# Kernel tuning notes

Hardware: AMD Instinct MI355X
Metric: run time of the kernel (lower is better)

The kernel has to match this reference:

```python
import jax, jax.numpy as jnp
import numpy as np

# env_params constants (chosen, see shape_source)
ETN, EAN = 64, 64          # entity type / attribute nums
RTN, RAN = 128, 64         # relationship type / attribute nums
ME, MR = 2048, 65536       # max entities / relationships
TES, THM, HID = 16, 256, 128
ENV = ETN + RTN + TES      # 208 = GRU input size


def _lin(key, out_d, in_d):
    k1, k2 = jax.random.split(key)
    lim = 1.0 / np.sqrt(in_d)
    W = jax.random.uniform(k1, (out_d, in_d), minval=-lim, maxval=lim, dtype=jnp.float32)
    b = jax.random.uniform(k2, (out_d,), minval=-lim, maxval=lim, dtype=jnp.float32)
    return W, b


def setup_inputs() -> dict:
    key = jax.random.key(0)
    ks = jax.random.split(key, 32)
    # entity: one-hot type in cols [0:ETN], random attributes after
    etype = jax.nn.one_hot(jax.random.randint(ks[0], (ME,), 0, ETN), ETN, dtype=jnp.float32)
    entity = jnp.concatenate([etype, jax.random.normal(ks[1], (ME, EAN), jnp.float32)], axis=1)
    rtype = jax.nn.one_hot(jax.random.randint(ks[2], (MR,), 0, RTN), RTN, dtype=jnp.float32)
    relationship = jnp.concatenate([rtype, jax.random.normal(ks[3], (MR, RAN + ME), jnp.float32)], axis=1)
    target = jax.random.normal(ks[4], (ME + EAN + MR + RAN,), jnp.float32)
    action_mask = (jax.random.uniform(ks[5], (THM,)) > 0.2).astype(jnp.float32)
    # entity encoder: 128 -> 32 -> 8 -> 1
    ew1, eb1 = _lin(ks[6], 32, ETN + EAN)
    ew2, eb2 = _lin(ks[7], 8, 32)
    ew3, eb3 = _lin(ks[8], 1, 8)
    # relationship encoder: 2240 -> 128 -> 64 -> 32 -> 8 -> 1
    rin = RTN + RAN + ME
    rw1, rb1 = _lin(ks[9], 128, rin)
    rw2, rb2 = _lin(ks[10], 64, 128)
    rw3, rb3 = _lin(ks[11], 32, 64)
    rw4, rb4 = _lin(ks[12], 8, 32)
    rw5, rb5 = _lin(ks[13], 1, 8)
    # target encoder: 67712 -> 64 -> 16
    tin = ME + EAN + MR + RAN
    tw1, tb1 = _lin(ks[14], 64, tin)
    tw2, tb2 = _lin(ks[15], TES, 64)
    # GRUCell(208, 128)
    lim = 1.0 / np.sqrt(HID)
    wih = jax.random.uniform(ks[16], (3 * HID, ENV), minval=-lim, maxval=lim, dtype=jnp.float32)
    whh = jax.random.uniform(ks[17], (3 * HID, HID), minval=-lim, maxval=lim, dtype=jnp.float32)
    bih = jax.random.uniform(ks[18], (3 * HID,), minval=-lim, maxval=lim, dtype=jnp.float32)
    bhh = jax.random.uniform(ks[19], (3 * HID,), minval=-lim, maxval=lim, dtype=jnp.float32)
    hidden = jax.random.normal(ks[20], (1, HID), jnp.float32)
    aw, ab = _lin(ks[21], THM, HID)
    return dict(entity=entity, relationship=relationship, target=target, action_mask=action_mask,
                ew1=ew1, eb1=eb1, ew2=ew2, eb2=eb2, ew3=ew3, eb3=eb3,
                rw1=rw1, rb1=rb1, rw2=rw2, rb2=rb2, rw3=rw3, rb3=rb3, rw4=rw4, rb4=rb4, rw5=rw5, rb5=rb5,
                tw1=tw1, tb1=tb1, tw2=tw2, tb2=tb2,
                wih=wih, whh=whh, bih=bih, bhh=bhh, hidden=hidden, aw=aw, ab=ab)


def _masked_group_max(onehot_mask, feat):
    # onehot_mask: [N, T] (==1 where row belongs to type t); feat: [N, 1]
    m = onehot_mask == 1.0
    vals = jnp.max(jnp.where(m, feat, -jnp.inf), axis=0)      # [T]
    return jnp.where(jnp.any(m, axis=0), vals, 0.0)            # empty group -> 0


def reference(entity, relationship, target, action_mask,
              ew1, eb1, ew2, eb2, ew3, eb3,
              rw1, rb1, rw2, rb2, rw3, rb3, rw4, rb4, rw5, rb5,
              tw1, tb1, tw2, tb2,
              wih, whh, bih, bhh, hidden, aw, ab):
    relu = jax.nn.relu
    # entity encoder -> [ME, 1]
    ef = relu(entity @ ew1.T + eb1)
    ef = relu(ef @ ew2.T + eb2)
    ef = ef @ ew3.T + eb3
    # relationship encoder -> [MR, 1]
    rf = relu(relationship @ rw1.T + rb1)
    rf = relu(rf @ rw2.T + rb2)
    rf = relu(rf @ rw3.T + rb3)
    rf = relu(rf @ rw4.T + rb4)
    rf = rf @ rw5.T + rb5
    # one-hot masked segment max over type columns
    eg = _masked_group_max(entity[:, :ETN], ef)          # [ETN]
    rg = _masked_group_max(relationship[:, :RTN], rf)    # [RTN]
    # target encoder -> [TES]
    tf = relu(target @ tw1.T + tb1) @ tw2.T + tb2
    env = jnp.concatenate([eg, rg, tf]).reshape(1, ENV)
    # GRUCell (torch gate order: r, z, n)
    gx = env @ wih.T + bih
    gh = hidden @ whh.T + bhh
    xr, xz, xn = jnp.split(gx, 3, axis=1)
    hr, hz, hn = jnp.split(gh, 3, axis=1)
    r = jax.nn.sigmoid(xr + hr)
    z = jax.nn.sigmoid(xz + hz)
    n = jnp.tanh(xn + r * hn)
    h = ((1.0 - z) * n + z * hidden).reshape(-1)         # [128]
    logits = jax.nn.softmax(h @ aw.T + ab, axis=0)       # [THM]
    return logits * action_mask
```

## Files before the change

### kernel.cpp

```cpp
#include <hip/hip_runtime.h>
#include <stdint.h>

typedef unsigned short u16;
typedef short s16x8 __attribute__((ext_vector_type(8)));
typedef float f32x4 __attribute__((ext_vector_type(4)));

__device__ __forceinline__ float bf2f(u16 u) {
  union { unsigned u; float f; } c; c.u = ((unsigned)u) << 16; return c.f;
}
__device__ __forceinline__ u16 f2bf(float f) {
  union { float f; unsigned u; } c; c.f = f;
  unsigned r = c.u + 0x7FFFu + ((c.u >> 16) & 1u);
  return (u16)(r >> 16);
}
__device__ __forceinline__ unsigned encf(float x) {
  union { float f; unsigned u; } c; c.f = x;
  return (c.u & 0x80000000u) ? ~c.u : (c.u | 0x80000000u);
}
__device__ __forceinline__ float decf(unsigned e) {
  union { unsigned u; float f; } c;
  c.u = (e & 0x80000000u) ? (e ^ 0x80000000u) : ~e;
  return c.f;
}
__device__ __forceinline__ f32x4 mfma16(s16x8 a, s16x8 b, f32x4 c) {
  return __builtin_amdgcn_mfma_f32_16x16x32_bf16(a, b, c, 0, 0, 0);
}
__device__ __forceinline__ float relu(float x) { return x > 0.f ? x : 0.f; }

template <int F32>
__device__ __forceinline__ void loadf8(const void* p, size_t ei, float* o) {
  if (F32) {
    const float* f = (const float*)p + ei;
    f32x4 a = *(const f32x4*)f;
    f32x4 b = *(const f32x4*)(f + 4);
#pragma unroll
    for (int j = 0; j < 4; ++j) { o[j] = a[j]; o[4 + j] = b[j]; }
  } else {
    s16x8 v = *(const s16x8*)((const u16*)p + ei);
#pragma unroll
    for (int j = 0; j < 8; ++j) o[j] = bf2f((u16)v[j]);
  }
}
template <int F32>
__device__ __forceinline__ s16x8 load8b(const void* p, size_t ei) {
  if (F32) {
    float o[8]; loadf8<1>(p, ei, o);
    s16x8 r;
#pragma unroll
    for (int j = 0; j < 8; ++j) r[j] = (short)f2bf(o[j]);
    return r;
  } else {
    return *(const s16x8*)((const u16*)p + ei);
  }
}
template <int F32>
__device__ __forceinline__ float ld1(const void* p, size_t ei) {
  return F32 ? ((const float*)p)[ei] : bf2f(((const u16*)p)[ei]);
}

__global__ void k_detect(const u16* __restrict__ entity, const u16* __restrict__ rel,
                         unsigned* __restrict__ ws) {
  __shared__ unsigned cnt[256];
  const int t = threadIdx.x;
  ws[t] = 0u;
  unsigned c = 0;
  for (int i = t; i < 16384; i += 256) {
    unsigned u = rel[i];
    if ((u & 0x7F80u) == 0x7F80u) ++c;
  }
  for (int i = t; i < 8192; i += 256) {
    unsigned u = entity[i];
    if ((u & 0x7F80u) == 0x7F80u) ++c;
  }
  cnt[t] = c;
  __syncthreads();
  for (int st = 128; st > 0; st >>= 1) {
    if (t < st) cnt[t] += cnt[t + st];
    __syncthreads();
  }
  if (t == 0) ws[256] = cnt[0] ? 1u : 0u;
}

template <int F32>
__global__ __launch_bounds__(256) void k_ent(
    const void* __restrict__ entity, const void* __restrict__ ew1, const void* __restrict__ eb1,
    const void* __restrict__ ew2, const void* __restrict__ eb2,
    const void* __restrict__ ew3, const void* __restrict__ eb3,
    unsigned* __restrict__ egws, const unsigned* __restrict__ flag) {
  if (*flag != (unsigned)F32) return;
  __shared__ __align__(16) u16 xl[32 * 136];
  __shared__ __align__(16) u16 w1l[32 * 136];
  __shared__ float h1l[32 * 33];
  __shared__ float h2l[32 * 9];
  const int t = threadIdx.x;
  const int row0 = blockIdx.x * 32;
#pragma unroll
  for (int p = 0; p < 2; ++p) {
    int lin = p * 256 + t, rr = lin >> 4, cc = lin & 15;
    *(s16x8*)(xl + rr * 136 + cc * 8) =
        load8b<F32>(entity, (size_t)(row0 + rr) * 128 + cc * 8);
    *(s16x8*)(w1l + rr * 136 + cc * 8) = load8b<F32>(ew1, (size_t)rr * 128 + cc * 8);
  }
  __syncthreads();
  {
    const int r = t >> 3, g = t & 7;
    float acc[4] = {0.f, 0.f, 0.f, 0.f};
#pragma unroll 4
    for (int c = 0; c < 16; ++c) {
      s16x8 xv = *(const s16x8*)(xl + r * 136 + c * 8);
      float xf[8];
#pragma unroll
      for (int j = 0; j < 8; ++j) xf[j] = bf2f((u16)xv[j]);
#pragma unroll
      for (int s = 0; s < 4; ++s) {
        s16x8 wv = *(const s16x8*)(w1l + (g + 8 * s) * 136 + c * 8);
#pragma unroll
        for (int j = 0; j < 8; ++j) acc[s] += xf[j] * bf2f((u16)wv[j]);
      }
    }
#pragma unroll
    for (int s = 0; s < 4; ++s)
      h1l[r * 33 + g + 8 * s] = relu(acc[s] + ld1<F32>(eb1, g + 8 * s));
  }
  __syncthreads();
  {
    const int r = t >> 3, o = t & 7;
    float a = ld1<F32>(eb2, o);
#pragma unroll 8
    for (int k = 0; k < 32; ++k) a += h1l[r * 33 + k] * ld1<F32>(ew2, o * 32 + k);
    h2l[r * 9 + o] = relu(a);
  }
  __syncthreads();
  if (t < 32) {
    float s = ld1<F32>(eb3, 0);
#pragma unroll
    for (int k = 0; k < 8; ++k) s += h2l[t * 9 + k] * ld1<F32>(ew3, k);
    int ty = 0;
#pragma unroll
    for (int c = 0; c < 8; ++c) {
      s16x8 v = *(const s16x8*)(xl + t * 136 + c * 8);
#pragma unroll
      for (int j = 0; j < 8; ++j)
        if ((u16)v[j] == (u16)0x3F80) ty = c * 8 + j;
    }
    atomicMax(egws + ty, encf(s));
  }
}

template <int F32>
__global__ __launch_bounds__(256) void k_tgt(const void* __restrict__ target,
                                             const void* __restrict__ tw1,
                                             float* __restrict__ tpart,
                                             const unsigned* __restrict__ flag) {
  if (*flag != (unsigned)F32) return;
  __shared__ float red[256];
  const int t = threadIdx.x;
  const int o = blockIdx.x >> 2, c = blockIdx.x & 3;
  float a = 0.f;
  for (int i = t; i < 2116; i += 256) {
    float xf[8], wf[8];
    loadf8<F32>(target, (size_t)c * 16928 + i * 8, xf);
    loadf8<F32>(tw1, (size_t)o * 67712 + c * 16928 + i * 8, wf);
#pragma unroll
    for (int j = 0; j < 8; ++j) a += xf[j] * wf[j];
  }
  red[t] = a;
  __syncthreads();
  for (int st = 128; st > 0; st >>= 1) {
    if (t < st) red[t] += red[t + st];
    __syncthreads();
  }
  if (t == 0) atomicAdd(tpart + o, red[0]);
}

#define RK 2240
template <int F32>
__global__ __launch_bounds__(256) void k_rel(
    const void* __restrict__ rel, const void* __restrict__ rw1, const void* __restrict__ rb1,
    const void* __restrict__ rw2, const void* __restrict__ rb2,
    const void* __restrict__ rw3, const void* __restrict__ rb3,
    const void* __restrict__ rw4, const void* __restrict__ rb4,
    const void* __restrict__ rw5, const void* __restrict__ rb5,
    unsigned* __restrict__ rgws, const unsigned* __restrict__ flag) {
  if (*flag != (unsigned)F32) return;
  __shared__ __align__(16) unsigned char sm[53760];
  u16* smA = (u16*)sm;
  u16* smB = (u16*)(sm + 8192);
  u16* r0 = (u16*)sm;
  u16* smRF = (u16*)(sm + 18432);
  int* styp = (int*)(sm + 53248);

  const int t = threadIdx.x;
  const int lane = t & 63;
  const int wid = t >> 6;
  const int row0 = blockIdx.x * 128;
  const int fr = lane & 15, fq = lane >> 4;

  if (t < 128) {
    int ty = 0;
#pragma unroll 4
    for (int c = 0; c < 16; ++c) {
      s16x8 v = load8b<F32>(rel, (size_t)(row0 + t) * RK + c * 8);
#pragma unroll
      for (int j = 0; j < 8; ++j)
        if ((u16)v[j] == (u16)0x3F80) ty = c * 8 + j;
    }
    styp[t] = ty;
  }

  const int wm = wid >> 1, wn = wid & 1;
  f32x4 acc[4][4];
#pragma unroll
  for (int i = 0; i < 4; ++i)
#pragma unroll
    for (int j = 0; j < 4; ++j) acc[i][j] = f32x4{0.f, 0.f, 0.f, 0.f};

  const size_t gA0 = (size_t)(row0 + (t >> 2)) * RK + (t & 3) * 8;
  const size_t gB0 = (size_t)(t >> 2) * RK + (t & 3) * 8;

  for (int ki = 0; ki < 70; ++ki) {
    const int k0 = ki * 32;
    s16x8 va0 = load8b<F32>(rel, gA0 + k0);
    s16x8 va1 = load8b<F32>(rel, gA0 + (size_t)64 * RK + k0);
    s16x8 vb0 = load8b<F32>(rw1, gB0 + k0);
    s16x8 vb1 = load8b<F32>(rw1, gB0 + (size_t)64 * RK + k0);
    __syncthreads();
    *(s16x8*)(smA + t * 8) = va0;
    *(s16x8*)(smA + 2048 + t * 8) = va1;
    *(s16x8*)(smB + t * 8) = vb0;
    *(s16x8*)(smB + 2048 + t * 8) = vb1;
    __syncthreads();
    s16x8 a[4], b[4];
#pragma unroll
    for (int i = 0; i < 4; ++i)
      a[i] = *(const s16x8*)(smA + (wm * 64 + i * 16 + fr) * 32 + fq * 8);
#pragma unroll
    for (int j = 0; j < 4; ++j)
      b[j] = *(const s16x8*)(smB + (wn * 64 + j * 16 + fr) * 32 + fq * 8);
#pragma unroll
    for (int i = 0; i < 4; ++i)
#pragma unroll
      for (int j = 0; j < 4; ++j) acc[i][j] = mfma16(a[i], b[j], acc[i][j]);
  }
  __syncthreads();

#pragma unroll
  for (int j = 0; j < 4; ++j) {
    const int col = wn * 64 + j * 16 + fr;
    const float bias = ld1<F32>(rb1, col);
#pragma unroll
    for (int i = 0; i < 4; ++i) {
      const int rbase = wm * 64 + i * 16 + fq * 4;
#pragma unroll
      for (int r = 0; r < 4; ++r)
        smRF[(rbase + r) * 136 + col] = f2bf(relu(acc[i][j][r] + bias));
    }
  }
  __syncthreads();

  if (t < 128) {
    const u16* rfrow = smRF + t * 136;
    for (int o = 0; o < 64; ++o) {
      float a = ld1<F32>(rb2, o);
      for (int k = 0; k < 128; k += 8) {
        float wf[8];
        loadf8<F32>(rw2, o * 128 + k, wf);
#pragma unroll
        for (int j = 0; j < 8; ++j) a += bf2f(rfrow[k + j]) * wf[j];
      }
      r0[t * 72 + o] = f2bf(relu(a));
    }
    const u16* h2row = r0 + t * 72;
    float h3[32];
#pragma unroll
    for (int o = 0; o < 32; ++o) {
      float a = ld1<F32>(rb3, o);
      for (int k = 0; k < 64; k += 8) {
        float wf[8];
        loadf8<F32>(rw3, o * 64 + k, wf);
#pragma unroll
        for (int j = 0; j < 8; ++j) a += bf2f(h2row[k + j]) * wf[j];
      }
      h3[o] = relu(a);
    }
    float h4[8];
#pragma unroll
    for (int o = 0; o < 8; ++o) {
      float a = ld1<F32>(rb4, o);
#pragma unroll
      for (int k = 0; k < 32; ++k) a += h3[k] * ld1<F32>(rw4, o * 32 + k);
      h4[o] = relu(a);
    }
    float s = ld1<F32>(rb5, 0);
#pragma unroll
    for (int k = 0; k < 8; ++k) s += h4[k] * ld1<F32>(rw5, k);
    atomicMax(rgws + styp[t], encf(s));
  }
}

__global__ __launch_bounds__(256, 2) void k_relf(
    const float* __restrict__ rel, const float* __restrict__ rw1, const float* __restrict__ rb1,
    const float* __restrict__ rw2, const float* __restrict__ rb2,
    const float* __restrict__ rw3, const float* __restrict__ rb3,
    const float* __restrict__ rw4, const float* __restrict__ rb4,
    const float* __restrict__ rw5, const float* __restrict__ rb5,
    unsigned* __restrict__ rgws, const unsigned* __restrict__ flag) {
  if (*flag != 1u) return;
  __shared__ __align__(16) unsigned char sm[53760];
  u16* r0 = (u16*)sm;
  u16* smRF = (u16*)(sm + 18432);

  const int t = threadIdx.x;
  const int lane = t & 63;
  const int wid = t >> 6;
  const int row0 = blockIdx.x * 128;
  const int fr = lane & 15, fq = lane >> 4;
  const int wm = wid >> 1, wn = wid & 1;

  int ty = 0;
  if (t < 128) {
    const float* rrow = rel + (size_t)(row0 + t) * RK;
#pragma unroll 8
    for (int c = 0; c < 128; c += 4) {
      f32x4 v = *(const f32x4*)(rrow + c);
#pragma unroll
      for (int j = 0; j < 4; ++j)
        if (v[j] == 1.0f) ty = c + j;
    }
  }

  f32x4 acc[4][4];
#pragma unroll
  for (int i = 0; i < 4; ++i)
#pragma unroll
    for (int j = 0; j < 4; ++j) acc[i][j] = f32x4{0.f, 0.f, 0.f, 0.f};

  const float* pa[4];
  const float* pb[4];
#pragma unroll
  for (int i = 0; i < 4; ++i) {
    pa[i] = rel + (size_t)(row0 + wm * 64 + i * 16 + fr) * RK + fq * 8;
    pb[i] = rw1 + (size_t)(wn * 64 + i * 16 + fr) * RK + fq * 8;
  }

#pragma unroll 2
  for (int ki = 0; ki < 70; ++ki) {
    f32x4 ar[4][2], br[4][2];
#pragma unroll
    for (int i = 0; i < 4; ++i) {
      ar[i][0] = *(const f32x4*)pa[i];
      ar[i][1] = *(const f32x4*)(pa[i] + 4);
      br[i][0] = *(const f32x4*)pb[i];
      br[i][1] = *(const f32x4*)(pb[i] + 4);
      pa[i] += 32;
      pb[i] += 32;
    }
    s16x8 af[4], bg[4];
#pragma unroll
    for (int i = 0; i < 4; ++i) {
#pragma unroll
      for (int e = 0; e < 4; ++e) {
        af[i][e] = (short)f2bf(ar[i][0][e]);
        af[i][4 + e] = (short)f2bf(ar[i][1][e]);
        bg[i][e] = (short)f2bf(br[i][0][e]);
        bg[i][4 + e] = (short)f2bf(br[i][1][e]);
      }
    }
#pragma unroll
    for (int i = 0; i < 4; ++i)
#pragma unroll
      for (int j = 0; j < 4; ++j) acc[i][j] = mfma16(af[i], bg[j], acc[i][j]);
  }

#pragma unroll
  for (int j = 0; j < 4; ++j) {
    const int col = wn * 64 + j * 16 + fr;
    const float bias = rb1[col];
#pragma unroll
    for (int i = 0; i < 4; ++i) {
      const int rbase = wm * 64 + i * 16 + fq * 4;
#pragma unroll
      for (int r = 0; r < 4; ++r)
        smRF[(rbase + r) * 136 + col] = f2bf(relu(acc[i][j][r] + bias));
    }
  }
  __syncthreads();

  if (t < 128) {
    const u16* rfrow = smRF + t * 136;
    for (int o = 0; o < 64; ++o) {
      float a = rb2[o];
      for (int k = 0; k < 128; k += 8) {
        f32x4 w0 = *(const f32x4*)(rw2 + o * 128 + k);
        f32x4 w1 = *(const f32x4*)(rw2 + o * 128 + k + 4);
#pragma unroll
        for (int j = 0; j < 4; ++j) {
          a += bf2f(rfrow[k + j]) * w0[j];
          a += bf2f(rfrow[k + 4 + j]) * w1[j];
        }
      }
      r0[t * 72 + o] = f2bf(relu(a));
    }
    const u16* h2row = r0 + t * 72;
    float h3[32];
#pragma unroll
    for (int o = 0; o < 32; ++o) {
      float a = rb3[o];
      for (int k = 0; k < 64; k += 8) {
        f32x4 w0 = *(const f32x4*)(rw3 + o * 64 + k);
        f32x4 w1 = *(const f32x4*)(rw3 + o * 64 + k + 4);
#pragma unroll
        for (int j = 0; j < 4; ++j) {
          a += bf2f(h2row[k + j]) * w0[j];
          a += bf2f(h2row[k + 4 + j]) * w1[j];
        }
      }
      h3[o] = relu(a);
    }
    float h4[8];
#pragma unroll
    for (int o = 0; o < 8; ++o) {
      float a = rb4[o];
#pragma unroll
      for (int k = 0; k < 32; ++k) a += h3[k] * rw4[o * 32 + k];
      h4[o] = relu(a);
    }
    float s = rb5[0];
#pragma unroll
    for (int k = 0; k < 8; ++k) s += h4[k] * rw5[k];
    atomicMax(rgws + ty, encf(s));
  }
}

template <int F32>
__global__ __launch_bounds__(256) void k_fin(
    const unsigned* __restrict__ egws, const unsigned* __restrict__ rgws,
    const float* __restrict__ tpart, const void* __restrict__ tb1,
    const void* __restrict__ tw2, const void* __restrict__ tb2,
    const void* __restrict__ wih, const void* __restrict__ whh,
    const void* __restrict__ bih, const void* __restrict__ bhh,
    const void* __restrict__ hidden, const void* __restrict__ aw,
    const void* __restrict__ ab, const void* __restrict__ amask,
    void* __restrict__ outp, const unsigned* __restrict__ flag) {
  if (*flag != (unsigned)F32) return;
  __shared__ float env[208];
  __shared__ float th1[64];
  __shared__ float gx[384], gh[384];
  __shared__ float hv[128], hid[128];
  __shared__ float red[256];
  const int t = threadIdx.x;
  if (t < 64) {
    unsigned e = egws[t];
    env[t] = e ? decf(e) : 0.f;
    th1[t] = relu(tpart[t] + ld1<F32>(tb1, t));
  }
  if (t >= 64 && t < 192) {
    unsigned e = rgws[t - 64];
    env[t] = e ? decf(e) : 0.f;
  }
  if (t < 128) hid[t] = ld1<F32>(hidden, t);
  __syncthreads();
  if (t < 16) {
    float a = ld1<F32>(tb2, t);
    for (int k = 0; k < 64; k += 8) {
      float wf[8];
      loadf8<F32>(tw2, t * 64 + k, wf);
#pragma unroll
      for (int j = 0; j < 8; ++j) a += th1[k + j] * wf[j];
    }
    env[192 + t] = a;
  }
  __syncthreads();
  for (int o = t; o < 384; o += 256) {
    float ax = ld1<F32>(bih, o);
#pragma unroll 2
    for (int c = 0; c < 26; ++c) {
      float wf[8];
      loadf8<F32>(wih, (size_t)o * 208 + c * 8, wf);
#pragma unroll
      for (int j = 0; j < 8; ++j) ax += env[c * 8 + j] * wf[j];
    }
    gx[o] = ax;
    float ah = ld1<F32>(bhh, o);
#pragma unroll 2
    for (int c = 0; c < 16; ++c) {
      float wf[8];
      loadf8<F32>(whh, (size_t)o * 128 + c * 8, wf);
#pragma unroll
      for (int j = 0; j < 8; ++j) ah += hid[c * 8 + j] * wf[j];
    }
    gh[o] = ah;
  }
  __syncthreads();
  if (t < 128) {
    float r = 1.f / (1.f + expf(-(gx[t] + gh[t])));
    float z = 1.f / (1.f + expf(-(gx[128 + t] + gh[128 + t])));
    float n = tanhf(gx[256 + t] + r * gh[256 + t]);
    hv[t] = (1.f - z) * n + z * hid[t];
  }
  __syncthreads();
  float s = ld1<F32>(ab, t);
#pragma unroll 4
  for (int c = 0; c < 16; ++c) {
    float wf[8];
    loadf8<F32>(aw, (size_t)t * 128 + c * 8, wf);
#pragma unroll
    for (int j = 0; j < 8; ++j) s += hv[c * 8 + j] * wf[j];
  }
  red[t] = s;
  __syncthreads();
  for (int st = 128; st > 0; st >>= 1) {
    if (t < st) red[t] = fmaxf(red[t], red[t + st]);
    __syncthreads();
  }
  float m = red[0];
  __syncthreads();
  float e = expf(s - m);
  red[t] = e;
  __syncthreads();
  for (int st = 128; st > 0; st >>= 1) {
    if (t < st) red[t] += red[t + st];
    __syncthreads();
  }
  float v = e * (1.f / red[0]) * ld1<F32>(amask, t);
  if (F32) ((float*)outp)[t] = v;
  else ((u16*)outp)[t] = f2bf(v);
}

extern "C" void kernel_launch(void* const* d_in, const int* in_sizes, int n_in,
                              void* d_out, int out_size, void* d_ws, size_t ws_size,
                              hipStream_t stream) {
  const void* entity = d_in[0];
  const void* rel    = d_in[1];
  const void* target = d_in[2];
  const void* amask  = d_in[3];
  const void* ew1 = d_in[4];  const void* eb1 = d_in[5];
  const void* ew2 = d_in[6];  const void* eb2 = d_in[7];
  const void* ew3 = d_in[8];  const void* eb3 = d_in[9];
  const void* rw1 = d_in[10]; const void* rb1 = d_in[11];
  const void* rw2 = d_in[12]; const void* rb2 = d_in[13];
  const void* rw3 = d_in[14]; const void* rb3 = d_in[15];
  const void* rw4 = d_in[16]; const void* rb4 = d_in[17];
  const void* rw5 = d_in[18]; const void* rb5 = d_in[19];
  const void* tw1 = d_in[20]; const void* tb1 = d_in[21];
  const void* tw2 = d_in[22]; const void* tb2 = d_in[23];
  const void* wih = d_in[24]; const void* whh = d_in[25];
  const void* bih = d_in[26]; const void* bhh = d_in[27];
  const void* hidden = d_in[28];
  const void* aw = d_in[29];  const void* ab = d_in[30];

  unsigned* ws = (unsigned*)d_ws;
  unsigned* egws = ws;
  unsigned* rgws = ws + 64;
  float* tpart = (float*)(ws + 192);
  const unsigned* flag = ws + 256;

  hipLaunchKernelGGL(k_detect, dim3(1), dim3(256), 0, stream,
                     (const u16*)entity, (const u16*)rel, ws);

  hipLaunchKernelGGL((k_ent<0>), dim3(64), dim3(256), 0, stream,
                     entity, ew1, eb1, ew2, eb2, ew3, eb3, egws, flag);
  hipLaunchKernelGGL((k_ent<1>), dim3(64), dim3(256), 0, stream,
                     entity, ew1, eb1, ew2, eb2, ew3, eb3, egws, flag);

  hipLaunchKernelGGL((k_tgt<0>), dim3(256), dim3(256), 0, stream, target, tw1, tpart, flag);
  hipLaunchKernelGGL((k_tgt<1>), dim3(256), dim3(256), 0, stream, target, tw1, tpart, flag);

  hipLaunchKernelGGL((k_rel<0>), dim3(512), dim3(256), 0, stream,
                     rel, rw1, rb1, rw2, rb2, rw3, rb3, rw4, rb4, rw5, rb5, rgws, flag);
  hipLaunchKernelGGL(k_relf, dim3(512), dim3(256), 0, stream,
                     (const float*)rel, (const float*)rw1, (const float*)rb1,
                     (const float*)rw2, (const float*)rb2, (const float*)rw3,
                     (const float*)rb3, (const float*)rw4, (const float*)rb4,
                     (const float*)rw5, (const float*)rb5, rgws, flag);

  hipLaunchKernelGGL((k_fin<0>), dim3(1), dim3(256), 0, stream,
                     egws, rgws, tpart, tb1, tw2, tb2, wih, whh, bih, bhh,
                     hidden, aw, ab, amask, d_out, flag);
  hipLaunchKernelGGL((k_fin<1>), dim3(1), dim3(256), 0, stream,
                     egws, rgws, tpart, tb1, tw2, tb2, wih, whh, bih, bhh,
                     hidden, aw, ab, amask, d_out, flag);
}
```

Measured before the change: 1.287 ms.

## Stage fp32 relationship GEMM tiles through double-buffered LDS as bf16

The fp32 relationship encoder kernel now has each thread load a contiguous 16-float chunk of A and B per K step, convert it to bf16 once, and store it into a double-buffered shared-memory tile. MFMA fragments are then read from LDS rather than each wave loading and converting its own strided global fragments. This removes redundant global loads and conversions across waves and lets the next tile's loads overlap the current tile's MFMAs. Type detection now reuses the staged bf16 tiles from the first four K steps instead of a separate global scan. The cost is more LDS per block and a barrier on every K step.

```diff
diff --git a/kernel.cpp b/kernel.cpp
--- a/kernel.cpp
+++ b/kernel.cpp
@@ -26,6 +26,15 @@
   return __builtin_amdgcn_mfma_f32_16x16x32_bf16(a, b, c, 0, 0, 0);
 }
 __device__ __forceinline__ float relu(float x) { return x > 0.f ? x : 0.f; }
+__device__ __forceinline__ s16x8 cvt8(f32x4 a, f32x4 b) {
+  s16x8 r;
+#pragma unroll
+  for (int e = 0; e < 4; ++e) {
+    r[e] = (short)f2bf(a[e]);
+    r[4 + e] = (short)f2bf(b[e]);
+  }
+  return r;
+}
 
 template <int F32>
 __device__ __forceinline__ void loadf8(const void* p, size_t ei, float* o) {
@@ -298,7 +307,7 @@
   }
 }
 
-__global__ __launch_bounds__(256, 2) void k_relf(
+__global__ __launch_bounds__(256, 2) void k_relg(
     const float* __restrict__ rel, const float* __restrict__ rw1, const float* __restrict__ rb1,
     const float* __restrict__ rw2, const float* __restrict__ rb2,
     const float* __restrict__ rw3, const float* __restrict__ rb3,
@@ -306,10 +315,7 @@
     const float* __restrict__ rw5, const float* __restrict__ rb5,
     unsigned* __restrict__ rgws, const unsigned* __restrict__ flag) {
   if (*flag != 1u) return;
-  __shared__ __align__(16) unsigned char sm[53760];
-  u16* r0 = (u16*)sm;
-  u16* smRF = (u16*)(sm + 18432);
-
+  __shared__ __align__(16) unsigned char sm[67584];
   const int t = threadIdx.x;
   const int lane = t & 63;
   const int wid = t >> 6;
@@ -317,61 +323,78 @@
   const int fr = lane & 15, fq = lane >> 4;
   const int wm = wid >> 1, wn = wid & 1;
 
+  const float* pA = rel + (size_t)(row0 + (t >> 1)) * RK + (t & 1) * 16;
+  const float* pB = rw1 + (size_t)(t >> 1) * RK + (t & 1) * 16;
+  const int sidx = 16 * t;
+
+  f32x4 acc[4][4];
+#pragma unroll
+  for (int i = 0; i < 4; ++i)
+#pragma unroll
+    for (int j = 0; j < 4; ++j) acc[i][j] = f32x4{0.f, 0.f, 0.f, 0.f};
+
+  {
+    f32x4 pre[8];
+#pragma unroll
+    for (int q = 0; q < 4; ++q) pre[q] = *(const f32x4*)(pA + q * 4);
+#pragma unroll
+    for (int q = 0; q < 4; ++q) pre[4 + q] = *(const f32x4*)(pB + q * 4);
+    u16* dA = (u16*)sm;
+    u16* dB = (u16*)(sm + 8192);
+    *(s16x8*)(dA + sidx) = cvt8(pre[0], pre[1]);
+    *(s16x8*)(dA + sidx + 8) = cvt8(pre[2], pre[3]);
+    *(s16x8*)(dB + sidx) = cvt8(pre[4], pre[5]);
+    *(s16x8*)(dB + sidx + 8) = cvt8(pre[6], pre[7]);
+  }
+  __syncthreads();
+
   int ty = 0;
-  if (t < 128) {
-    const float* rrow = rel + (size_t)(row0 + t) * RK;
-#pragma unroll 8
-    for (int c = 0; c < 128; c += 4) {
-      f32x4 v = *(const f32x4*)(rrow + c);
-#pragma unroll
-      for (int j = 0; j < 4; ++j)
-        if (v[j] == 1.0f) ty = c + j;
-    }
-  }
-
-  f32x4 acc[4][4];
-#pragma unroll
-  for (int i = 0; i < 4; ++i)
-#pragma unroll
-    for (int j = 0; j < 4; ++j) acc[i][j] = f32x4{0.f, 0.f, 0.f, 0.f};
-
-  const float* pa[4];
-  const float* pb[4];
-#pragma unroll
-  for (int i = 0; i < 4; ++i) {
-    pa[i] = rel + (size_t)(row0 + wm * 64 + i * 16 + fr) * RK + fq * 8;
-    pb[i] = rw1 + (size_t)(wn * 64 + i * 16 + fr) * RK + fq * 8;
-  }
-
-#pragma unroll 2
+#pragma unroll 1
   for (int ki = 0; ki < 70; ++ki) {
-    f32x4 ar[4][2], br[4][2];
-#pragma unroll
-    for (int i = 0; i < 4; ++i) {
-      ar[i][0] = *(const f32x4*)pa[i];
-      ar[i][1] = *(const f32x4*)(pa[i] + 4);
-      br[i][0] = *(const f32x4*)pb[i];
-      br[i][1] = *(const f32x4*)(pb[i] + 4);
-      pa[i] += 32;
-      pb[i] += 32;
-    }
-    s16x8 af[4], bg[4];
-#pragma unroll
-    for (int i = 0; i < 4; ++i) {
-#pragma unroll
-      for (int e = 0; e < 4; ++e) {
-        af[i][e] = (short)f2bf(ar[i][0][e]);
-        af[i][4 + e] = (short)f2bf(ar[i][1][e]);
-        bg[i][e] = (short)f2bf(br[i][0][e]);
-        bg[i][4 + e] = (short)f2bf(br[i][1][e]);
+    const int nk = ki + 1;
+    f32x4 pre[8];
+    if (nk < 70) {
+      const int k0 = nk * 32;
+#pragma unroll
+      for (int q = 0; q < 4; ++q) pre[q] = *(const f32x4*)(pA + k0 + q * 4);
+#pragma unroll
+      for (int q = 0; q < 4; ++q) pre[4 + q] = *(const f32x4*)(pB + k0 + q * 4);
+    }
+    const u16* bA = (const u16*)(sm + (ki & 1) * 16384);
+    const u16* bB = (const u16*)(sm + (ki & 1) * 16384 + 8192);
+    s16x8 a[4], b[4];
+#pragma unroll
+    for (int i = 0; i < 4; ++i)
+      a[i] = *(const s16x8*)(bA + (wm * 64 + i * 16 + fr) * 32 + fq * 8);
+#pragma unroll
+    for (int j = 0; j < 4; ++j)
+      b[j] = *(const s16x8*)(bB + (wn * 64 + j * 16 + fr) * 32 + fq * 8);
+#pragma unroll
+    for (int i = 0; i < 4; ++i)
+#pragma unroll
+      for (int j = 0; j < 4; ++j) acc[i][j] = mfma16(a[i], b[j], acc[i][j]);
+    if (ki < 4 && t < 128) {
+#pragma unroll
+      for (int c = 0; c < 4; ++c) {
+        s16x8 v = *(const s16x8*)(bA + t * 32 + c * 8);
+#pragma unroll
+        for (int j = 0; j < 8; ++j)
+          if ((u16)v[j] == (u16)0x3F80) ty = ki * 32 + c * 8 + j;
       }
     }
-#pragma unroll
-    for (int i = 0; i < 4; ++i)
-#pragma unroll
-      for (int j = 0; j < 4; ++j) acc[i][j] = mfma16(af[i], bg[j], acc[i][j]);
-  }
-
+    if (nk < 70) {
+      u16* dA = (u16*)(sm + (nk & 1) * 16384);
+      u16* dB = (u16*)(sm + (nk & 1) * 16384 + 8192);
+      *(s16x8*)(dA + sidx) = cvt8(pre[0], pre[1]);
+      *(s16x8*)(dA + sidx + 8) = cvt8(pre[2], pre[3]);
+      *(s16x8*)(dB + sidx) = cvt8(pre[4], pre[5]);
+      *(s16x8*)(dB + sidx + 8) = cvt8(pre[6], pre[7]);
+    }
+    __syncthreads();
+  }
+
+  u16* smRF = (u16*)(sm + 32768);
+  u16* r0 = (u16*)sm;
 #pragma unroll
   for (int j = 0; j < 4; ++j) {
     const int col = wn * 64 + j * 16 + fr;
@@ -391,13 +414,10 @@
     for (int o = 0; o < 64; ++o) {
       float a = rb2[o];
       for (int k = 0; k < 128; k += 8) {
-        f32x4 w0 = *(const f32x4*)(rw2 + o * 128 + k);
-        f32x4 w1 = *(const f32x4*)(rw2 + o * 128 + k + 4);
-#pragma unroll
-        for (int j = 0; j < 4; ++j) {
-          a += bf2f(rfrow[k + j]) * w0[j];
-          a += bf2f(rfrow[k + 4 + j]) * w1[j];
-        }
+        float wf[8];
+        loadf8<1>(rw2, (size_t)o * 128 + k, wf);
+#pragma unroll
+        for (int j = 0; j < 8; ++j) a += bf2f(rfrow[k + j]) * wf[j];
       }
       r0[t * 72 + o] = f2bf(relu(a));
     }
@@ -407,13 +427,10 @@
     for (int o = 0; o < 32; ++o) {
       float a = rb3[o];
       for (int k = 0; k < 64; k += 8) {
-        f32x4 w0 = *(const f32x4*)(rw3 + o * 64 + k);
-        f32x4 w1 = *(const f32x4*)(rw3 + o * 64 + k + 4);
-#pragma unroll
-        for (int j = 0; j < 4; ++j) {
-          a += bf2f(h2row[k + j]) * w0[j];
-          a += bf2f(h2row[k + 4 + j]) * w1[j];
-        }
+        float wf[8];
+        loadf8<1>(rw3, (size_t)o * 64 + k, wf);
+#pragma unroll
+        for (int j = 0; j < 8; ++j) a += bf2f(h2row[k + j]) * wf[j];
       }
       h3[o] = relu(a);
     }
@@ -568,7 +585,7 @@
 
   hipLaunchKernelGGL((k_rel<0>), dim3(512), dim3(256), 0, stream,
                      rel, rw1, rb1, rw2, rb2, rw3, rb3, rw4, rb4, rw5, rb5, rgws, flag);
-  hipLaunchKernelGGL(k_relf, dim3(512), dim3(256), 0, stream,
+  hipLaunchKernelGGL(k_relg, dim3(512), dim3(256), 0, stream,
                      (const float*)rel, (const float*)rw1, (const float*)rb1,
                      (const float*)rw2, (const float*)rb2, (const float*)rw3,
                      (const float*)rb3, (const float*)rw4, (const float*)rb4,
```

Measured after the change: 1.102 ms. -14.3%, faster.
